# Optimization experiments

Measured on AMD Instinct MI355X. Metric: run time of the kernel, lower is better.

The kernel has to match this reference:

```python
import jax, jax.numpy as jnp
import numpy as np

H, D = 16, 1024
HD = D // H  # 64

def setup_inputs() -> dict:
    key = jax.random.key(0)
    ks = jax.random.split(key, 11)
    B, S = 2, 2048
    s_in = 1.0 / np.sqrt(D)
    return {
        "V": jax.random.normal(ks[0], (B, S, D), jnp.float32),
        "K": jax.random.normal(ks[1], (B, S, D), jnp.float32),
        "Q": jax.random.normal(ks[2], (B, S, D), jnp.float32),
        # stacked per-head Linear weights, torch layout [out,in] -> [H, HD, D]
        "Wv": jax.random.normal(ks[3], (H, HD, D), jnp.float32) * s_in,
        "bv": jnp.zeros((H, HD), jnp.float32),
        "Wk": jax.random.normal(ks[4], (H, HD, D), jnp.float32) * s_in,
        "bk": jnp.zeros((H, HD), jnp.float32),
        "Wq": jax.random.normal(ks[5], (H, HD, D), jnp.float32) * s_in,
        "bq": jnp.zeros((H, HD), jnp.float32),
        "Wo": jax.random.normal(ks[6], (D, D), jnp.float32) * s_in,
        "bo": jnp.zeros((D,), jnp.float32),
    }

def reference(V, K, Q, Wv, bv, Wk, bk, Wq, bq, Wo, bo):
    scale = HD ** (-0.5)
    # per-head projections fused into one batched GEMM: [B,S,D] x [H,HD,D] -> [B,H,S,HD]
    q = jnp.einsum('bsd,hed->bhse', Q, Wq) + bq[None, :, None, :]
    k = jnp.einsum('bsd,hed->bhse', K, Wk) + bk[None, :, None, :]
    v = jnp.einsum('bsd,hed->bhse', V, Wv) + bv[None, :, None, :]
    # scaled dot-product attention
    scores = jnp.einsum('bhqe,bhke->bhqk', q, k) * scale  # [B,H,S,S]
    p = jax.nn.softmax(scores, axis=-1)
    att = jnp.einsum('bhqk,bhke->bhqe', p, v)  # [B,H,S,HD]
    # concat heads (head 0 first, matching the torch cat order) then output proj
    B, _, S, _ = att.shape
    cat = jnp.transpose(att, (0, 2, 1, 3)).reshape(B, S, H * HD)
    return cat @ Wo.T + bo
```

## Files before the change

kernel.cpp:

```cpp
#include <hip/hip_runtime.h>
#include <cstdint>
#include <cstddef>

typedef __bf16 bf16_t;
typedef bf16_t bf16x8 __attribute__((ext_vector_type(8)));
typedef bf16_t bf16x4 __attribute__((ext_vector_type(4)));
typedef float f32x4 __attribute__((ext_vector_type(4)));
typedef float f32x2 __attribute__((ext_vector_type(2)));

__device__ __forceinline__ void gl_lds16(const void* g, void* l) {
  __builtin_amdgcn_global_load_lds(
      (const __attribute__((address_space(1))) void*)g,
      (__attribute__((address_space(3))) void*)l, 16, 0, 0);
}

__device__ __forceinline__ f32x4 mfma16(bf16x8 a, bf16x8 b, f32x4 c) {
  return __builtin_amdgcn_mfma_f32_16x16x32_bf16(a, b, c, 0, 0, 0);
}

__device__ __forceinline__ float exp2_fast(float x) {
  float r;
  asm("v_exp_f32 %0, %1" : "=v"(r) : "v"(x));
  return r;
}

#define SCHED_FENCE() __builtin_amdgcn_sched_barrier(0)
#define WAIT_VM0()   do { asm volatile("s_waitcnt vmcnt(0)");   SCHED_FENCE(); } while (0)
#define WAIT_LGKM0() do { asm volatile("s_waitcnt lgkmcnt(0)"); SCHED_FENCE(); } while (0)
#define RAW_BAR()    do { __builtin_amdgcn_s_barrier();         SCHED_FENCE(); } while (0)

struct CvtArgs { const float* src[7]; bf16_t* dst[7]; };

__global__ __launch_bounds__(256) void convert_all(CvtArgs a) {
  unsigned g = blockIdx.x * 256u + threadIdx.x;
  unsigned seg, off;
  if (g < 524288u) {
    seg = g >> 17; off = g & 131071u;
  } else {
    unsigned h = g - 524288u;
    seg = 4u + (h >> 19); off = h & 524287u;
  }
  const float4* s = (const float4*)a.src[seg] + (size_t)off * 2;
  float4 x0 = s[0], x1 = s[1];
  bf16x8 o;
  o[0] = (bf16_t)x0.x; o[1] = (bf16_t)x0.y; o[2] = (bf16_t)x0.z; o[3] = (bf16_t)x0.w;
  o[4] = (bf16_t)x1.x; o[5] = (bf16_t)x1.y; o[6] = (bf16_t)x1.z; o[7] = (bf16_t)x1.w;
  *(bf16x8*)(a.dst[seg] + (size_t)off * 8) = o;
}

__device__ __forceinline__ void stage128(const bf16_t* src, bf16_t* dst, int t, int w) {
  #pragma unroll
  for (int i = 0; i < 4; i++) {
    int g = t + i * 256;
    int r = g >> 3, pc = g & 7;
    int lc = pc ^ (r & 7);
    gl_lds16(src + (size_t)r * 1024 + lc * 8, dst + i * 2048 + w * 512);
  }
}
__device__ __forceinline__ void stage64(const bf16_t* src, bf16_t* dst, int t, int w) {
  #pragma unroll
  for (int i = 0; i < 2; i++) {
    int g = t + i * 256;
    int r = g >> 3, pc = g & 7;
    int lc = pc ^ (r & 7);
    gl_lds16(src + (size_t)r * 1024 + lc * 8, dst + i * 2048 + w * 512);
  }
}

struct ProjArgs {
  const bf16_t* A[3]; const bf16_t* W[3]; const float* bias[3];
  bf16_t* out[3]; float scale[3];
};

__global__ __launch_bounds__(256, 2) void gemm_proj(ProjArgs p) {
  __shared__ __attribute__((aligned(16))) unsigned char smem[65536];
  const int z = blockIdx.z;
  const bf16_t* A = p.A[z] + (size_t)blockIdx.x * 128 * 1024;
  const bf16_t* W = p.W[z] + (size_t)blockIdx.y * 128 * 1024;

  const int t = threadIdx.x;
  const int w = t >> 6, l = t & 63;
  const int lq = l >> 4, lr = l & 15;
  const int mq = w & 1, nq = w >> 1;

  f32x4 acc[4][4];
  f32x4 zero = {0.f, 0.f, 0.f, 0.f};
  #pragma unroll
  for (int i = 0; i < 4; i++)
    #pragma unroll
    for (int j = 0; j < 4; j++) acc[i][j] = zero;

  stage128(A, (bf16_t*)smem, t, w);
  stage128(W, (bf16_t*)(smem + 16384), t, w);
  WAIT_VM0();
  RAW_BAR();

  for (int step = 0; step < 16; ++step) {
    const int cur = step & 1;
    bf16_t* as = (bf16_t*)(smem + cur * 32768);
    bf16_t* bs = (bf16_t*)(smem + cur * 32768 + 16384);
    if (step < 15) {
      bf16_t* an = (bf16_t*)(smem + (cur ^ 1) * 32768);
      stage128(A + (step + 1) * 64, an, t, w);
      stage128(W + (step + 1) * 64, an + 8192, t, w);
    }
    SCHED_FENCE();
    #pragma unroll
    for (int kk = 0; kk < 2; kk++) {
      bf16x8 af[4], bfr[4];
      #pragma unroll
      for (int i = 0; i < 4; i++) {
        int R = mq * 64 + i * 16 + lr;
        int ch = (kk * 4 + lq) ^ (R & 7);
        af[i] = *(const bf16x8*)(as + R * 64 + ch * 8);
      }
      #pragma unroll
      for (int j = 0; j < 4; j++) {
        int R = nq * 64 + j * 16 + lr;
        int ch = (kk * 4 + lq) ^ (R & 7);
        bfr[j] = *(const bf16x8*)(bs + R * 64 + ch * 8);
      }
      __builtin_amdgcn_s_setprio(1);
      #pragma unroll
      for (int i = 0; i < 4; i++)
        #pragma unroll
        for (int j = 0; j < 4; j++)
          acc[i][j] = mfma16(af[i], bfr[j], acc[i][j]);
      __builtin_amdgcn_s_setprio(0);
    }
    WAIT_VM0();
    RAW_BAR();
  }

  const float* bias = p.bias[z];
  const float scale = p.scale[z];
  __syncthreads();
  bf16_t* ts = (bf16_t*)smem;
  #pragma unroll
  for (int i = 0; i < 4; i++) {
    #pragma unroll
    for (int j = 0; j < 4; j++) {
      int nl = nq * 64 + j * 16 + lr;
      float bz = bias[blockIdx.y * 128 + nl];
      #pragma unroll
      for (int r = 0; r < 4; r++) {
        int ml = mq * 64 + i * 16 + lq * 4 + r;
        bf16_t val = (bf16_t)((acc[i][j][r] + bz) * scale);
        if (z == 0) {
          int mlp = (ml & 96) | (((ml >> 2) & 3) << 3) | (((ml >> 4) & 1) << 2) | (ml & 3);
          ts[nl * 136 + mlp] = val;
        } else {
          ts[ml * 136 + nl] = val;
        }
      }
    }
  }
  __syncthreads();
  bf16_t* out = p.out[z];
  const int b = blockIdx.x >> 4, sbase = (blockIdx.x & 15) * 128;
  if (z == 0) {
    #pragma unroll
    for (int ii = 0; ii < 8; ii++) {
      int idx = t * 8 + ii * 2048;
      int rr = idx >> 7, cc = idx & 127;
      int n = blockIdx.y * 128 + rr;
      int h = n >> 6, e = n & 63;
      bf16x8 vq = *(const bf16x8*)(ts + rr * 136 + cc);
      *(bf16x8*)(out + ((size_t)(b * 16 + h) * 64 + e) * 2048 + sbase + cc) = vq;
    }
  } else {
    #pragma unroll
    for (int ii = 0; ii < 8; ii++) {
      int idx = t * 8 + ii * 2048;
      int rr = idx >> 7, cc = idx & 127;
      int n = blockIdx.y * 128 + cc;
      int h = n >> 6, e = n & 63;
      bf16x8 vq = *(const bf16x8*)(ts + rr * 136 + cc);
      *(bf16x8*)(out + ((size_t)(b * 16 + h) * 2048 + sbase + rr) * 64 + e) = vq;
    }
  }
}

__global__ __launch_bounds__(256, 2) void attn(
    const bf16_t* __restrict__ qw, const bf16_t* __restrict__ kw,
    const bf16_t* __restrict__ vtw, bf16_t* __restrict__ att)
{
  __shared__ __attribute__((aligned(16))) unsigned char smem[49152];
  const int bh = blockIdx.x, qt = blockIdx.y;
  const int t = threadIdx.x, w = t >> 6, l = t & 63, lq = l >> 4, lr = l & 15;

  const bf16_t* kb0 = kw + (size_t)bh * 131072;
  const bf16_t* vb0 = vtw + (size_t)bh * 131072;
  bf16_t* qstage = (bf16_t*)(smem + 32768);

  const bf16_t* qbase = qw + ((size_t)bh * 2048 + qt * 128) * 64;
  #pragma unroll
  for (int i = 0; i < 4; i++) {
    int g = t + i * 256;
    int r = g >> 3, pc = g & 7;
    int lc = pc ^ (r & 7);
    gl_lds16(qbase + (size_t)r * 64 + lc * 8, qstage + i * 2048 + w * 512);
  }
  #pragma unroll
  for (int tt = 0; tt < 2; tt++) {
    bf16_t* kn = (bf16_t*)(smem + tt * 16384);
    const bf16_t* kbase = kb0 + (size_t)tt * 4096;
    const bf16_t* vbase = vb0 + (size_t)tt * 64;
    #pragma unroll
    for (int i = 0; i < 2; i++) {
      int g = t + i * 256;
      int r = g >> 3, pc = g & 7;
      int lc = pc ^ (r & 7);
      gl_lds16(kbase + (size_t)r * 64 + lc * 8, kn + i * 2048 + w * 512);
      gl_lds16(vbase + (size_t)r * 2048 + lc * 8, kn + 4096 + i * 2048 + w * 512);
    }
  }
  asm volatile("s_waitcnt vmcnt(8)");
  SCHED_FENCE();
  RAW_BAR();
  bf16x8 qf[2][2];
  #pragma unroll
  for (int gq = 0; gq < 2; gq++)
    #pragma unroll
    for (int kk = 0; kk < 2; kk++) {
      int R = w * 32 + gq * 16 + lr;
      int ch = (kk * 4 + lq) ^ (R & 7);
      qf[gq][kk] = *(const bf16x8*)(qstage + R * 64 + ch * 8);
    }
  asm volatile("s_waitcnt vmcnt(4) lgkmcnt(0)");
  SCHED_FENCE();
  RAW_BAR();

  f32x4 O[2][4];
  f32x4 zero = {0.f, 0.f, 0.f, 0.f};
  #pragma unroll
  for (int gq = 0; gq < 2; gq++)
    #pragma unroll
    for (int et = 0; et < 4; et++) O[gq][et] = zero;
  f32x2 lsv[2];
  lsv[0] = f32x2{0.f, 0.f}; lsv[1] = f32x2{0.f, 0.f};
  bf16x8 vfA[8], vfB[8];
  bf16x8 pbA[2][2], pbB[2][2];

#define ATTN_BODY(KT, BUF, NBUF, PBOUT, PBIN, VFOUT, VFIN, FIRST, DOSTAGE, ENDWAIT) \
  {                                                                              \
    bf16_t* ksb = (bf16_t*)(smem + (BUF) * 16384);                               \
    bf16_t* vsb = (bf16_t*)(smem + (BUF) * 16384 + 8192);                        \
    if (DOSTAGE) {                                                               \
      bf16_t* kn = (bf16_t*)(smem + (NBUF) * 16384);                             \
      const bf16_t* kbase = kb0 + (size_t)((KT) + 2) * 4096;                     \
      const bf16_t* vbase = vb0 + (size_t)((KT) + 2) * 64;                       \
      _Pragma("unroll")                                                          \
      for (int i = 0; i < 2; i++) {                                              \
        int g = t + i * 256;                                                     \
        int r = g >> 3, pc = g & 7;                                              \
        int lc = pc ^ (r & 7);                                                   \
        gl_lds16(kbase + (size_t)r * 64 + lc * 8, kn + i * 2048 + w * 512);      \
        gl_lds16(vbase + (size_t)r * 2048 + lc * 8, kn + 4096 + i * 2048 + w * 512); \
      }                                                                          \
    }                                                                            \
    SCHED_FENCE();                                                               \
    f32x4 sc[2][4];                                                              \
    _Pragma("unroll")                                                            \
    for (int gq = 0; gq < 2; gq++)                                               \
      _Pragma("unroll")                                                          \
      for (int j = 0; j < 4; j++) sc[gq][j] = zero;                              \
    __builtin_amdgcn_s_setprio(1);                                               \
    if (!(FIRST)) {                                                              \
      _Pragma("unroll")                                                          \
      for (int ks2 = 0; ks2 < 2; ks2++)                                          \
        _Pragma("unroll")                                                        \
        for (int et = 0; et < 4; et++) {                                         \
          O[0][et] = mfma16((VFIN)[ks2 * 4 + et], (PBIN)[0][ks2], O[0][et]);     \
          O[1][et] = mfma16((VFIN)[ks2 * 4 + et], (PBIN)[1][ks2], O[1][et]);     \
        }                                                                        \
    }                                                                            \
    _Pragma("unroll")                                                            \
    for (int kk = 0; kk < 2; kk++)                                               \
      _Pragma("unroll")                                                          \
      for (int j = 0; j < 4; j++) {                                              \
        int R = j * 16 + lr;                                                     \
        int ch = (kk * 4 + lq) ^ (R & 7);                                        \
        bf16x8 kf = *(const bf16x8*)(ksb + R * 64 + ch * 8);                     \
        sc[0][j] = mfma16(kf, qf[0][kk], sc[0][j]);                              \
        sc[1][j] = mfma16(kf, qf[1][kk], sc[1][j]);                              \
      }                                                                          \
    __builtin_amdgcn_s_setprio(0);                                               \
    _Pragma("unroll")                                                            \
    for (int ks2 = 0; ks2 < 2; ks2++)                                            \
      _Pragma("unroll")                                                          \
      for (int et = 0; et < 4; et++) {                                           \
        int R = et * 16 + lr;                                                    \
        int ch = (ks2 * 4 + lq) ^ (R & 7);                                       \
        (VFOUT)[ks2 * 4 + et] = *(const bf16x8*)(vsb + R * 64 + ch * 8);         \
      }                                                                          \
    _Pragma("unroll")                                                            \
    for (int gq = 0; gq < 2; gq++)                                               \
      _Pragma("unroll")                                                          \
      for (int ks2 = 0; ks2 < 2; ks2++)                                          \
        _Pragma("unroll")                                                        \
        for (int r = 0; r < 4; r++) {                                            \
          float e0 = exp2_fast(sc[gq][2 * ks2][r]);                              \
          float e1 = exp2_fast(sc[gq][2 * ks2 + 1][r]);                          \
          f32x2 ee = {e0, e1};                                                   \
          lsv[gq] += ee;                                                         \
          (PBOUT)[gq][ks2][r] = (bf16_t)e0;                                      \
          (PBOUT)[gq][ks2][4 + r] = (bf16_t)e1;                                  \
        }                                                                        \
          \
          \
    asm volatile("s_waitcnt vmcnt(" ENDWAIT ") lgkmcnt(0)");                     \
    SCHED_FENCE();                                                               \
    RAW_BAR();                                                                   \
  }

  ATTN_BODY(0, 0, 2, pbA, pbB, vfA, vfB, true,  true, "4");
  ATTN_BODY(1, 1, 0, pbB, pbA, vfB, vfA, false, true, "4");
  ATTN_BODY(2, 2, 1, pbA, pbB, vfA, vfB, false, true, "4");
  ATTN_BODY(3, 0, 2, pbB, pbA, vfB, vfA, false, true, "4");
  ATTN_BODY(4, 1, 0, pbA, pbB, vfA, vfB, false, true, "4");
  ATTN_BODY(5, 2, 1, pbB, pbA, vfB, vfA, false, true, "4");
  for (int g6 = 6; g6 < 30; g6 += 6) {
    ATTN_BODY(g6 + 0, 0, 2, pbA, pbB, vfA, vfB, false, true, "4");
    ATTN_BODY(g6 + 1, 1, 0, pbB, pbA, vfB, vfA, false, true, "4");
    ATTN_BODY(g6 + 2, 2, 1, pbA, pbB, vfA, vfB, false, true, "4");
    ATTN_BODY(g6 + 3, 0, 2, pbB, pbA, vfB, vfA, false, true, "4");
    ATTN_BODY(g6 + 4, 1, 0, pbA, pbB, vfA, vfB, false, true, "4");
    ATTN_BODY(g6 + 5, 2, 1, pbB, pbA, vfB, vfA, false, true, "4");
  }
  ATTN_BODY(30, 0, 2, pbA, pbB, vfA, vfB, false, false, "0");
  ATTN_BODY(31, 1, 0, pbB, pbA, vfB, vfA, false, false, "0");
#undef ATTN_BODY

  #pragma unroll
  for (int ks2 = 0; ks2 < 2; ks2++)
    #pragma unroll
    for (int et = 0; et < 4; et++) {
      O[0][et] = mfma16(vfB[ks2 * 4 + et], pbB[0][ks2], O[0][et]);
      O[1][et] = mfma16(vfB[ks2 * 4 + et], pbB[1][ks2], O[1][et]);
    }

  float s0 = lsv[0][0] + lsv[0][1];
  float s1 = lsv[1][0] + lsv[1][1];
  s0 += __shfl_xor(s0, 16);
  s0 += __shfl_xor(s0, 32);
  s1 += __shfl_xor(s1, 16);
  s1 += __shfl_xor(s1, 32);
  float rinv[2] = {1.0f / s0, 1.0f / s1};

  bf16_t* ts = (bf16_t*)smem;
  #pragma unroll
  for (int gq = 0; gq < 2; gq++)
    #pragma unroll
    for (int et = 0; et < 4; et++) {
      bf16x4 pv;
      #pragma unroll
      for (int r = 0; r < 4; r++) pv[r] = (bf16_t)(O[gq][et][r] * rinv[gq]);
      *(bf16x4*)(ts + (w * 32 + gq * 16 + lr) * 72 + et * 16 + lq * 4) = pv;
    }
  __syncthreads();
  const int b = bh >> 4, h = bh & 15;
  #pragma unroll
  for (int i = 0; i < 4; i++) {
    int c = t + i * 256;
    int row = c >> 3, c8 = c & 7;
    bf16x8 vv = *(const bf16x8*)(ts + row * 72 + c8 * 8);
    *(bf16x8*)(att + ((size_t)b * 2048 + qt * 128 + row) * 1024 + h * 64 + c8 * 8) = vv;
  }
}

__global__ __launch_bounds__(256, 3) void gemm_out(
    const bf16_t* __restrict__ A, const bf16_t* __restrict__ W,
    const float* __restrict__ bias, float* __restrict__ out)
{
  __shared__ __attribute__((aligned(16))) unsigned char smem[49152];
  const bf16_t* Ab = A + (size_t)blockIdx.x * 64 * 1024;
  const bf16_t* Wb = W + (size_t)blockIdx.y * 128 * 1024;
  const int t = threadIdx.x, w = t >> 6, l = t & 63, lq = l >> 4, lr = l & 15;
  const int mh = w & 1, nh = w >> 1;

  f32x4 acc[2][4];
  f32x4 zero = {0.f, 0.f, 0.f, 0.f};
  #pragma unroll
  for (int i = 0; i < 2; i++)
    #pragma unroll
    for (int j = 0; j < 4; j++) acc[i][j] = zero;

  stage64(Ab, (bf16_t*)smem, t, w);
  stage128(Wb, (bf16_t*)(smem + 8192), t, w);
  WAIT_VM0();
  RAW_BAR();

  for (int step = 0; step < 16; ++step) {
    const int cur = step & 1;
    bf16_t* as = (bf16_t*)(smem + cur * 24576);
    bf16_t* bs = (bf16_t*)(smem + cur * 24576 + 8192);
    if (step < 15) {
      bf16_t* an = (bf16_t*)(smem + (cur ^ 1) * 24576);
      stage64(Ab + (step + 1) * 64, an, t, w);
      stage128(Wb + (step + 1) * 64, an + 4096, t, w);
    }
    SCHED_FENCE();
    #pragma unroll
    for (int kk = 0; kk < 2; kk++) {
      bf16x8 af[2], bfr[4];
      #pragma unroll
      for (int i = 0; i < 2; i++) {
        int R = mh * 32 + i * 16 + lr;
        int ch = (kk * 4 + lq) ^ (R & 7);
        af[i] = *(const bf16x8*)(as + R * 64 + ch * 8);
      }
      #pragma unroll
      for (int j = 0; j < 4; j++) {
        int R = nh * 64 + j * 16 + lr;
        int ch = (kk * 4 + lq) ^ (R & 7);
        bfr[j] = *(const bf16x8*)(bs + R * 64 + ch * 8);
      }
      __builtin_amdgcn_s_setprio(1);
      #pragma unroll
      for (int i = 0; i < 2; i++)
        #pragma unroll
        for (int j = 0; j < 4; j++)
          acc[i][j] = mfma16(af[i], bfr[j], acc[i][j]);
      __builtin_amdgcn_s_setprio(0);
    }
    WAIT_VM0();
    RAW_BAR();
  }

  #pragma unroll
  for (int i = 0; i < 2; i++) {
    #pragma unroll
    for (int j = 0; j < 4; j++) {
      int col = blockIdx.y * 128 + nh * 64 + j * 16 + lr;
      float bz = bias[col];
      #pragma unroll
      for (int r = 0; r < 4; r++) {
        int row = blockIdx.x * 64 + mh * 32 + i * 16 + lq * 4 + r;
        out[(size_t)row * 1024 + col] = acc[i][j][r] + bz;
      }
    }
  }
}

extern "C" void kernel_launch(void* const* d_in, const int* in_sizes, int n_in,
                              void* d_out, int out_size, void* d_ws, size_t ws_size,
                              hipStream_t stream) {
  (void)in_sizes; (void)n_in; (void)out_size;
  const float* V  = (const float*)d_in[0];
  const float* Kx = (const float*)d_in[1];
  const float* Q  = (const float*)d_in[2];
  const float* Wv = (const float*)d_in[3];
  const float* bv = (const float*)d_in[4];
  const float* Wk = (const float*)d_in[5];
  const float* bk = (const float*)d_in[6];
  const float* Wq = (const float*)d_in[7];
  const float* bq = (const float*)d_in[8];
  const float* Wo = (const float*)d_in[9];
  const float* bo = (const float*)d_in[10];

  const size_t E = 1048576;
  if (ws_size < 20 * E * sizeof(bf16_t)) return;

  bf16_t* ws = (bf16_t*)d_ws;
  bf16_t* cWo   = ws;
  bf16_t* cWv   = ws + E;
  bf16_t* cWk   = ws + 2 * E;
  bf16_t* cWq   = ws + 3 * E;
  bf16_t* q_ws  = ws + 4 * E;
  bf16_t* k_ws  = ws + 8 * E;
  bf16_t* vt_ws = ws + 12 * E;
  bf16_t* att_ws= ws + 16 * E;

  bf16_t* cV = att_ws;
  bf16_t* cK = (bf16_t*)d_out;
  bf16_t* cQ = (bf16_t*)d_out + 4 * E;

  CvtArgs ca;
  ca.src[0] = Wo; ca.src[1] = Wv; ca.src[2] = Wk; ca.src[3] = Wq;
  ca.src[4] = V;  ca.src[5] = Kx; ca.src[6] = Q;
  ca.dst[0] = cWo; ca.dst[1] = cWv; ca.dst[2] = cWk; ca.dst[3] = cWq;
  ca.dst[4] = cV;  ca.dst[5] = cK;  ca.dst[6] = cQ;
  convert_all<<<8192, 256, 0, stream>>>(ca);

  ProjArgs pa;
  pa.A[0] = cV;  pa.A[1] = cK;  pa.A[2] = cQ;
  pa.W[0] = cWv; pa.W[1] = cWk; pa.W[2] = cWq;
  pa.bias[0] = bv; pa.bias[1] = bk; pa.bias[2] = bq;
  pa.out[0] = vt_ws; pa.out[1] = k_ws; pa.out[2] = q_ws;
  pa.scale[0] = 1.f; pa.scale[1] = 1.f; pa.scale[2] = 0.125f * 1.4426950408889634f;
  gemm_proj<<<dim3(32, 8, 3), 256, 0, stream>>>(pa);

  attn<<<dim3(32, 16), 256, 0, stream>>>(q_ws, k_ws, vt_ws, att_ws);

  gemm_out<<<dim3(64, 8), 256, 0, stream>>>(att_ws, cWo, bo, (float*)d_out);
}
```

Measured before the change: 204.7 us.

## Triple-buffer projection and output GEMMs with BK=32 tiles and partial vmcnt waits

Both GEMM kernels move from a double-buffered K=64 pipeline to a triple-buffered K=32 pipeline. Each step stages a tile two steps ahead and waits only for the older loads via partial vmcnt counts, so global loads overlap more with MFMA work. The new paired-row swizzled LDS layout cuts shared memory per block, which lets gemm_proj run 3 blocks per CU. In exchange there are twice as many barriers and steps, fewer MFMAs per barrier, and gemm_out's launch bound drops to 2 blocks per CU.

```diff
diff --git a/kernel.cpp b/kernel.cpp
--- a/kernel.cpp
+++ b/kernel.cpp
@@ -57,14 +57,27 @@
     gl_lds16(src + (size_t)r * 1024 + lc * 8, dst + i * 2048 + w * 512);
   }
 }
-__device__ __forceinline__ void stage64(const bf16_t* src, bf16_t* dst, int t, int w) {
+__device__ __forceinline__ void stage128x32(const bf16_t* src, bf16_t* dst, int t, int w) {
   #pragma unroll
   for (int i = 0; i < 2; i++) {
     int g = t + i * 256;
-    int r = g >> 3, pc = g & 7;
-    int lc = pc ^ (r & 7);
-    gl_lds16(src + (size_t)r * 1024 + lc * 8, dst + i * 2048 + w * 512);
-  }
+    int rp = g >> 3, pc = g & 7;
+    int lc = pc ^ (rp & 7);
+    int R = rp * 2 + (lc >> 2), c4 = lc & 3;
+    gl_lds16(src + (size_t)R * 1024 + c4 * 8, dst + i * 2048 + w * 512);
+  }
+}
+__device__ __forceinline__ void stage64x32(const bf16_t* src, bf16_t* dst, int t, int w) {
+  int g = t;
+  int rp = g >> 3, pc = g & 7;
+  int lc = pc ^ (rp & 7);
+  int R = rp * 2 + (lc >> 2), c4 = lc & 3;
+  gl_lds16(src + (size_t)R * 1024 + c4 * 8, dst + w * 512);
+}
+__device__ __forceinline__ bf16x8 frag32(const bf16_t* buf, int R, int lq) {
+  int rp = R >> 1;
+  int pc = ((R & 1) * 4 + lq) ^ (rp & 7);
+  return *(const bf16x8*)(buf + rp * 64 + pc * 8);
 }
 
 struct ProjArgs {
@@ -72,8 +85,8 @@
   bf16_t* out[3]; float scale[3];
 };
 
-__global__ __launch_bounds__(256, 2) void gemm_proj(ProjArgs p) {
-  __shared__ __attribute__((aligned(16))) unsigned char smem[65536];
+__global__ __launch_bounds__(256, 3) void gemm_proj(ProjArgs p) {
+  __shared__ __attribute__((aligned(16))) unsigned char smem[49152];
   const int z = blockIdx.z;
   const bf16_t* A = p.A[z] + (size_t)blockIdx.x * 128 * 1024;
   const bf16_t* W = p.W[z] + (size_t)blockIdx.y * 128 * 1024;
@@ -90,47 +103,49 @@
     #pragma unroll
     for (int j = 0; j < 4; j++) acc[i][j] = zero;
 
-  stage128(A, (bf16_t*)smem, t, w);
-  stage128(W, (bf16_t*)(smem + 16384), t, w);
-  WAIT_VM0();
+  stage128x32(A,      (bf16_t*)smem,                t, w);
+  stage128x32(W,      (bf16_t*)(smem + 8192),       t, w);
+  stage128x32(A + 32, (bf16_t*)(smem + 16384),      t, w);
+  stage128x32(W + 32, (bf16_t*)(smem + 16384 + 8192), t, w);
+  asm volatile("s_waitcnt vmcnt(4)");
+  SCHED_FENCE();
   RAW_BAR();
 
-  for (int step = 0; step < 16; ++step) {
-    const int cur = step & 1;
-    bf16_t* as = (bf16_t*)(smem + cur * 32768);
-    bf16_t* bs = (bf16_t*)(smem + cur * 32768 + 16384);
-    if (step < 15) {
-      bf16_t* an = (bf16_t*)(smem + (cur ^ 1) * 32768);
-      stage128(A + (step + 1) * 64, an, t, w);
-      stage128(W + (step + 1) * 64, an + 8192, t, w);
-    }
-    SCHED_FENCE();
-    #pragma unroll
-    for (int kk = 0; kk < 2; kk++) {
-      bf16x8 af[4], bfr[4];
-      #pragma unroll
-      for (int i = 0; i < 4; i++) {
-        int R = mq * 64 + i * 16 + lr;
-        int ch = (kk * 4 + lq) ^ (R & 7);
-        af[i] = *(const bf16x8*)(as + R * 64 + ch * 8);
-      }
-      #pragma unroll
-      for (int j = 0; j < 4; j++) {
-        int R = nq * 64 + j * 16 + lr;
-        int ch = (kk * 4 + lq) ^ (R & 7);
-        bfr[j] = *(const bf16x8*)(bs + R * 64 + ch * 8);
-      }
-      __builtin_amdgcn_s_setprio(1);
-      #pragma unroll
-      for (int i = 0; i < 4; i++)
-        #pragma unroll
-        for (int j = 0; j < 4; j++)
-          acc[i][j] = mfma16(af[i], bfr[j], acc[i][j]);
-      __builtin_amdgcn_s_setprio(0);
-    }
-    WAIT_VM0();
-    RAW_BAR();
-  }
+#define PROJ_STEP(KT, BUF, NBUF, DOSTAGE, WAITN)                                 \
+  {                                                                              \
+    bf16_t* as = (bf16_t*)(smem + (BUF) * 16384);                                \
+    bf16_t* bs = (bf16_t*)(smem + (BUF) * 16384 + 8192);                         \
+    if (DOSTAGE) {                                                               \
+      bf16_t* an = (bf16_t*)(smem + (NBUF) * 16384);                             \
+      stage128x32(A + ((KT) + 2) * 32, an, t, w);                                \
+      stage128x32(W + ((KT) + 2) * 32, an + 4096, t, w);                         \
+    }                                                                            \
+    SCHED_FENCE();                                                               \
+    bf16x8 af[4], bfr[4];                                                        \
+    _Pragma("unroll")                                                            \
+    for (int i = 0; i < 4; i++) af[i] = frag32(as, mq * 64 + i * 16 + lr, lq);   \
+    _Pragma("unroll")                                                            \
+    for (int j = 0; j < 4; j++) bfr[j] = frag32(bs, nq * 64 + j * 16 + lr, lq);  \
+    __builtin_amdgcn_s_setprio(1);                                               \
+    _Pragma("unroll")                                                            \
+    for (int i = 0; i < 4; i++)                                                  \
+      _Pragma("unroll")                                                          \
+      for (int j = 0; j < 4; j++)                                                \
+        acc[i][j] = mfma16(af[i], bfr[j], acc[i][j]);                            \
+    __builtin_amdgcn_s_setprio(0);                                               \
+    asm volatile("s_waitcnt vmcnt(" WAITN ") lgkmcnt(0)");                       \
+    SCHED_FENCE();                                                               \
+    RAW_BAR();                                                                   \
+  }
+
+  for (int k3 = 0; k3 < 30; k3 += 3) {
+    PROJ_STEP(k3 + 0, 0, 2, true, "4");
+    PROJ_STEP(k3 + 1, 1, 0, true, "4");
+    PROJ_STEP(k3 + 2, 2, 1, true, "4");
+  }
+  PROJ_STEP(30, 0, 2, false, "0");
+  PROJ_STEP(31, 1, 0, false, "0");
+#undef PROJ_STEP
 
   const float* bias = p.bias[z];
   const float scale = p.scale[z];
@@ -369,11 +384,11 @@
   }
 }
 
-__global__ __launch_bounds__(256, 3) void gemm_out(
+__global__ __launch_bounds__(256, 2) void gemm_out(
     const bf16_t* __restrict__ A, const bf16_t* __restrict__ W,
     const float* __restrict__ bias, float* __restrict__ out)
 {
-  __shared__ __attribute__((aligned(16))) unsigned char smem[49152];
+  __shared__ __attribute__((aligned(16))) unsigned char smem[36864];
   const bf16_t* Ab = A + (size_t)blockIdx.x * 64 * 1024;
   const bf16_t* Wb = W + (size_t)blockIdx.y * 128 * 1024;
   const int t = threadIdx.x, w = t >> 6, l = t & 63, lq = l >> 4, lr = l & 15;
@@ -386,47 +401,49 @@
     #pragma unroll
     for (int j = 0; j < 4; j++) acc[i][j] = zero;
 
-  stage64(Ab, (bf16_t*)smem, t, w);
-  stage128(Wb, (bf16_t*)(smem + 8192), t, w);
-  WAIT_VM0();
+  stage64x32 (Ab,      (bf16_t*)smem,                 t, w);
+  stage128x32(Wb,      (bf16_t*)(smem + 4096),        t, w);
+  stage64x32 (Ab + 32, (bf16_t*)(smem + 12288),       t, w);
+  stage128x32(Wb + 32, (bf16_t*)(smem + 12288 + 4096), t, w);
+  asm volatile("s_waitcnt vmcnt(3)");
+  SCHED_FENCE();
   RAW_BAR();
 
-  for (int step = 0; step < 16; ++step) {
-    const int cur = step & 1;
-    bf16_t* as = (bf16_t*)(smem + cur * 24576);
-    bf16_t* bs = (bf16_t*)(smem + cur * 24576 + 8192);
-    if (step < 15) {
-      bf16_t* an = (bf16_t*)(smem + (cur ^ 1) * 24576);
-      stage64(Ab + (step + 1) * 64, an, t, w);
-      stage128(Wb + (step + 1) * 64, an + 4096, t, w);
-    }
-    SCHED_FENCE();
-    #pragma unroll
-    for (int kk = 0; kk < 2; kk++) {
-      bf16x8 af[2], bfr[4];
-      #pragma unroll
-      for (int i = 0; i < 2; i++) {
-        int R = mh * 32 + i * 16 + lr;
-        int ch = (kk * 4 + lq) ^ (R & 7);
-        af[i] = *(const bf16x8*)(as + R * 64 + ch * 8);
-      }
-      #pragma unroll
-      for (int j = 0; j < 4; j++) {
-        int R = nh * 64 + j * 16 + lr;
-        int ch = (kk * 4 + lq) ^ (R & 7);
-        bfr[j] = *(const bf16x8*)(bs + R * 64 + ch * 8);
-      }
-      __builtin_amdgcn_s_setprio(1);
-      #pragma unroll
-      for (int i = 0; i < 2; i++)
-        #pragma unroll
-        for (int j = 0; j < 4; j++)
-          acc[i][j] = mfma16(af[i], bfr[j], acc[i][j]);
-      __builtin_amdgcn_s_setprio(0);
-    }
-    WAIT_VM0();
-    RAW_BAR();
-  }
+#define OUT_STEP(KT, BUF, NBUF, DOSTAGE, WAITN)                                  \
+  {                                                                              \
+    bf16_t* as = (bf16_t*)(smem + (BUF) * 12288);                                \
+    bf16_t* bs = (bf16_t*)(smem + (BUF) * 12288 + 4096);                         \
+    if (DOSTAGE) {                                                               \
+      bf16_t* an = (bf16_t*)(smem + (NBUF) * 12288);                             \
+      stage64x32 (Ab + ((KT) + 2) * 32, an, t, w);                               \
+      stage128x32(Wb + ((KT) + 2) * 32, an + 2048, t, w);                        \
+    }                                                                            \
+    SCHED_FENCE();                                                               \
+    bf16x8 af[2], bfr[4];                                                        \
+    _Pragma("unroll")                                                            \
+    for (int i = 0; i < 2; i++) af[i] = frag32(as, mh * 32 + i * 16 + lr, lq);   \
+    _Pragma("unroll")                                                            \
+    for (int j = 0; j < 4; j++) bfr[j] = frag32(bs, nh * 64 + j * 16 + lr, lq);  \
+    __builtin_amdgcn_s_setprio(1);                                               \
+    _Pragma("unroll")                                                            \
+    for (int i = 0; i < 2; i++)                                                  \
+      _Pragma("unroll")                                                          \
+      for (int j = 0; j < 4; j++)                                                \
+        acc[i][j] = mfma16(af[i], bfr[j], acc[i][j]);                            \
+    __builtin_amdgcn_s_setprio(0);                                               \
+    asm volatile("s_waitcnt vmcnt(" WAITN ") lgkmcnt(0)");                       \
+    SCHED_FENCE();                                                               \
+    RAW_BAR();                                                                   \
+  }
+
+  for (int k3 = 0; k3 < 30; k3 += 3) {
+    OUT_STEP(k3 + 0, 0, 2, true, "3");
+    OUT_STEP(k3 + 1, 1, 0, true, "3");
+    OUT_STEP(k3 + 2, 2, 1, true, "3");
+  }
+  OUT_STEP(30, 0, 2, false, "0");
+  OUT_STEP(31, 1, 0, false, "0");
+#undef OUT_STEP
 
   #pragma unroll
   for (int i = 0; i < 2; i++) {
```

Result: no change. 201.4 us (-1.6%).
